# Kernel optimization log

Measured on AMD Instinct MI355X. Metric: run time of the kernel, lower is better.

## Reference

```python
import jax, jax.numpy as jnp
from jax import lax
import numpy as np

RADIUS = 2.0
K = 32          # max_neighbors
KNN = 3         # knn_num for FP interpolation
DEPTH = 3
NH = 16         # nhidden
NIN = 16
NOUT = 2
N = 16384
BOX = 32.0


def sqdist(a, b):
    # a: [M,3], b: [N,3] -> [M,N] squared distances (no [M,N,3] intermediate)
    d2 = (jnp.sum(a * a, -1)[:, None] + jnp.sum(b * b, -1)[None, :]
          - 2.0 * a @ b.T)
    return jnp.maximum(d2, 0.0)


def fps(pos, m):
    # farthest point sampling, deterministic start at index 0 (eval mode)
    n = pos.shape[0]
    def step(carry, _):
        mind, last = carry
        d = jnp.sum((pos - pos[last]) ** 2, axis=-1)
        mind = jnp.minimum(mind, d)
        nxt = jnp.argmax(mind).astype(jnp.int32)
        return (mind, nxt), nxt
    init = (jnp.full((n,), jnp.inf, dtype=pos.dtype), jnp.array(0, jnp.int32))
    _, rest = lax.scan(step, init, None, length=m - 1)
    return jnp.concatenate([jnp.zeros((1,), jnp.int32), rest])


def radius_group(pos_tgt, pos_src, r, k):
    # up-to-k neighbors of each target within radius r (nearest-first)
    d2 = sqdist(pos_tgt, pos_src)                      # [M,N]
    neg = jnp.where(d2 <= r * r, -d2, -jnp.inf)
    vals, cols = lax.top_k(neg, k)                     # [M,K]
    valid = jnp.isfinite(vals)
    return cols, valid


def knn_interpolate(x_c, pos_c, pos_f, k):
    d2 = sqdist(pos_f, pos_c)                          # [Nf, Nc]
    negv, nn = lax.top_k(-d2, k)                       # k nearest coarse pts
    w = 1.0 / jnp.maximum(-negv, 1e-16)
    w = w / jnp.sum(w, -1, keepdims=True)
    return jnp.sum(x_c[nn] * w[..., None], axis=1)     # [Nf, C]


def mlp2(h, W0, b0, W1, b1, act_last=True):
    h = jax.nn.relu(h @ W0 + b0)
    h = h @ W1 + b1
    return jax.nn.relu(h) if act_last else h


def setup_inputs() -> dict:
    key = jax.random.key(0)
    ks = jax.random.split(key, 24)
    s = 0.2
    dim_sa = NH + 3   # 19: PointConv concat(x_j, rel_pos)
    dim_fp = NH + NH  # 32: FP concat(interp, skip)
    return {
        "x": jax.random.normal(ks[0], (N, NIN), jnp.float32),
        "pos": jax.random.uniform(ks[1], (N, 3), jnp.float32) * BOX,
        "batch": jnp.zeros((N,), jnp.int32),
        "lin_in_W0": jax.random.normal(ks[2], (NIN, NH)) * s,
        "lin_in_b0": jnp.zeros((NH,), jnp.float32),
        "lin_in_W1": jax.random.normal(ks[3], (NH, NH)) * s,
        "lin_in_b1": jnp.zeros((NH,), jnp.float32),
        "sa_W0": jax.random.normal(ks[4], (DEPTH, dim_sa, dim_sa)) * s,
        "sa_b0": jnp.zeros((DEPTH, dim_sa), jnp.float32),
        "sa_W1": jax.random.normal(ks[5], (DEPTH, dim_sa, NH)) * s,
        "sa_b1": jnp.zeros((DEPTH, NH), jnp.float32),
        "fp_W0": jax.random.normal(ks[6], (DEPTH, dim_fp, dim_fp)) * s,
        "fp_b0": jnp.zeros((DEPTH, dim_fp), jnp.float32),
        "fp_W1": jax.random.normal(ks[7], (DEPTH, dim_fp, NH)) * s,
        "fp_b1": jnp.zeros((DEPTH, NH), jnp.float32),
        "lo_W0": jax.random.normal(ks[8], (NH, NH)) * s,
        "lo_b0": jnp.zeros((NH,), jnp.float32),
        "lo_W1": jax.random.normal(ks[9], (NH, NOUT)) * s,
        "lo_b1": jnp.zeros((NOUT,), jnp.float32),
    }


def reference(x, pos, batch,
              lin_in_W0, lin_in_b0, lin_in_W1, lin_in_b1,
              sa_W0, sa_b0, sa_W1, sa_b1,
              fp_W0, fp_b0, fp_W1, fp_b1,
              lo_W0, lo_b0, lo_W1, lo_b1):
    # lin_in MLP
    h = mlp2(x, lin_in_W0, lin_in_b0, lin_in_W1, lin_in_b1)
    sa = [(h, pos)]
    # SA (downsampling) path
    for i in range(DEPTH):
        xi, pi = sa[i]
        m = pi.shape[0] // 2                      # ratio = 0.5
        idx = fps(pi, m)
        pt = pi[idx]                              # sampled centers [M,3]
        cols, valid = radius_group(pt, pi, RADIUS, K)   # [M,K]
        xj = xi[cols]                             # [M,K,NH]
        rel = pi[cols] - pt[:, None, :]           # [M,K,3]
        msg = jnp.concatenate([xj, rel], -1)      # [M,K,19]
        msg = mlp2(msg, sa_W0[i], sa_b0[i], sa_W1[i], sa_b1[i])
        msg = jnp.where(valid[..., None], msg, -1e30)
        xn = jnp.max(msg, axis=1)                 # max aggregation (PointConv)
        sa.append((xn, pt))
    # FP (upsampling) path
    xf, pf = sa[DEPTH]
    for i in range(DEPTH - 1, -1, -1):
        xs, ps = sa[i]
        xi = knn_interpolate(xf, pf, ps, KNN)
        hcat = jnp.concatenate([xi, xs], -1)      # [Nf, 32]
        xf = mlp2(hcat, fp_W0[i], fp_b0[i], fp_W1[i], fp_b1[i])
        pf = ps
    # lin_out: relu then linear (act=['relu', None])
    return mlp2(xf, lo_W0, lo_b0, lo_W1, lo_b1, act_last=False)
```

## Files before the change

kernel.cpp:

```cpp
#include <hip/hip_runtime.h>
#include <stdint.h>


#define DEV static __device__ __forceinline__

DEV float fadd_(float a, float b){ return __fadd_rn(a,b); }
DEV float fsub_(float a, float b){ return __fsub_rn(a,b); }
DEV float fmul_(float a, float b){ return __fmul_rn(a,b); }
DEV float fdiv_(float a, float b){ return __fdiv_rn(a,b); }

DEV float dot3(float ax,float ay,float az,float bx,float by,float bz){
  return fmaf(az,bz, fmaf(ay,by, __fmul_rn(ax,bx)));
}
DEV float sqd(float na, float nb, float d){
  float t = __fadd_rn(na, nb);
  float u = __fmul_rn(2.0f, d);
  return fmaxf(__fsub_rn(t, u), 0.0f);
}

DEV float bbd2(float sx,float sy,float sz,
               float lx,float ly,float lz,float hx,float hy,float hz){
  float dx = fmaxf(fmaxf(fsub_(lx,sx), fsub_(sx,hx)), 0.0f);
  float dy = fmaxf(fmaxf(fsub_(ly,sy), fsub_(sy,hy)), 0.0f);
  float dz = fmaxf(fmaxf(fsub_(lz,sz), fsub_(sz,hz)), 0.0f);
  return fadd_(fadd_(fmul_(dx,dx),fmul_(dy,dy)),fmul_(dz,dz));
}

#define DPP0(src, ctrl, rm, bc) \
  __builtin_amdgcn_update_dpp(0, (int)(src), (ctrl), (rm), 0xf, (bc))

#define DPP64(dst, src, ctrl, rm, bc) { \
  uint32_t lo_ = (uint32_t)DPP0((uint32_t)(src), ctrl, rm, bc); \
  uint32_t hi_ = (uint32_t)DPP0((uint32_t)((src)>>32), ctrl, rm, bc); \
  (dst) = (((unsigned long long)hi_)<<32) | lo_; }

#define MERGE2(A1, A2, ctrl, rm, bc) { \
  unsigned long long b1_, b2_, mn_, mx_; \
  DPP64(b1_, A1, ctrl, rm, bc); \
  DPP64(b2_, A2, ctrl, rm, bc); \
  mn_ = (A1) < b1_ ? (A1) : b1_; \
  mx_ = (A2) > b2_ ? (A2) : b2_; \
  (A1) = (A1) > b1_ ? (A1) : b1_; \
  (A2) = mn_ > mx_ ? mn_ : mx_; }

DEV unsigned long long rdlane64(unsigned long long v, int l){
  uint32_t lo=(uint32_t)__builtin_amdgcn_readlane((int)(uint32_t)v, l);
  uint32_t hi=(uint32_t)__builtin_amdgcn_readlane((int)(uint32_t)(v>>32), l);
  return (((unsigned long long)hi)<<32)|lo;
}

DEV void wtop2(unsigned long long &A1, unsigned long long &A2){
  MERGE2(A1,A2,0x111,0xf,true)
  MERGE2(A1,A2,0x112,0xf,true)
  MERGE2(A1,A2,0x114,0xf,true)
  MERGE2(A1,A2,0x118,0xf,true)
  MERGE2(A1,A2,0x142,0xa,false)
  MERGE2(A1,A2,0x143,0xc,false)
  A1 = rdlane64(A1,63); A2 = rdlane64(A2,63);
}
DEV void htop2(unsigned long long &A1, unsigned long long &A2){
  MERGE2(A1,A2,0x111,0xf,true)
  MERGE2(A1,A2,0x112,0xf,true)
  MERGE2(A1,A2,0x114,0xf,true)
  MERGE2(A1,A2,0x118,0xf,true)
  MERGE2(A1,A2,0x142,0xa,false)
  A1 = rdlane64(A1,31); A2 = rdlane64(A2,31);
}

__global__ __launch_bounds__(256) void k_prep(
    const float* __restrict__ x, const float* __restrict__ pos,
    const float* __restrict__ W0, const float* __restrict__ b0,
    const float* __restrict__ W1, const float* __restrict__ b1,
    float4* __restrict__ pos4, float* __restrict__ h_out, int n)
{
  __shared__ float sW0[256], sb0[16], sW1[256], sb1[16];
  int tid = threadIdx.x;
  sW0[tid] = W0[tid];
  sW1[tid] = W1[tid];
  if (tid < 16){ sb0[tid] = b0[tid]; sb1[tid] = b1[tid]; }
  __syncthreads();
  int p = blockIdx.x*256 + tid;
  if (p >= n) return;

  float px = pos[3*p], py = pos[3*p+1], pz = pos[3*p+2];
  float nrm = fadd_(fadd_(fmul_(px,px), fmul_(py,py)), fmul_(pz,pz));
  pos4[p] = make_float4(px,py,pz,nrm);

  const float4* xr = (const float4*)(x + (size_t)p*16);
  float4 v0 = xr[0], v1 = xr[1], v2 = xr[2], v3 = xr[3];
  float xin[16] = {v0.x,v0.y,v0.z,v0.w, v1.x,v1.y,v1.z,v1.w,
                   v2.x,v2.y,v2.z,v2.w, v3.x,v3.y,v3.z,v3.w};
  float h1[16];
  #pragma unroll
  for (int o=0;o<16;o++){
    float acc = fmul_(xin[0], sW0[o]);
    #pragma unroll
    for (int k=1;k<16;k++) acc = fmaf(xin[k], sW0[k*16+o], acc);
    h1[o] = fmaxf(fadd_(acc, sb0[o]), 0.0f);
  }
  float h2[16];
  #pragma unroll
  for (int o=0;o<16;o++){
    float acc = fmul_(h1[0], sW1[o]);
    #pragma unroll
    for (int k=1;k<16;k++) acc = fmaf(h1[k], sW1[k*16+o], acc);
    h2[o] = fmaxf(fadd_(acc, sb1[o]), 0.0f);
  }
  float4* hw = (float4*)(h_out + (size_t)p*16);
  hw[0] = make_float4(h2[0], h2[1], h2[2], h2[3]);
  hw[1] = make_float4(h2[4], h2[5], h2[6], h2[7]);
  hw[2] = make_float4(h2[8], h2[9], h2[10],h2[11]);
  hw[3] = make_float4(h2[12],h2[13],h2[14],h2[15]);
}

DEV uint32_t expand4(uint32_t v){
  return (v&1u) | ((v&2u)<<2) | ((v&4u)<<4) | ((v&8u)<<6);
}
DEV int cellc(float v){
  int c = (int)(v*0.5f);
  return c < 0 ? 0 : (c > 15 ? 15 : c);
}
DEV uint32_t mkey(float4 p){
  return expand4((uint32_t)cellc(p.x))
       | (expand4((uint32_t)cellc(p.y))<<1)
       | (expand4((uint32_t)cellc(p.z))<<2);
}

__global__ __launch_bounds__(1024) void k_sort(
  const float4* __restrict__ nat, float4* __restrict__ srt,
  int* __restrict__ rank0, int n)
{
  __shared__ uint32_t hist[4096];
  __shared__ uint32_t gsum[1024];
  int tid = threadIdx.x;
  for (int i=tid;i<4096;i+=1024) hist[i]=0u;
  __syncthreads();
  for (int i=tid;i<n;i+=1024){
    float4 p = nat[i];
    atomicAdd(&hist[mkey(p)], 1u);
  }
  __syncthreads();
  uint32_t h0=hist[4*tid],h1=hist[4*tid+1],h2=hist[4*tid+2],h3=hist[4*tid+3];
  gsum[tid] = h0+h1+h2+h3;
  __syncthreads();
  for (int off=1; off<1024; off<<=1){
    uint32_t v = gsum[tid];
    uint32_t a = (tid>=off)? gsum[tid-off] : 0u;
    __syncthreads();
    gsum[tid] = v + a;
    __syncthreads();
  }
  uint32_t excl = (tid>0)? gsum[tid-1] : 0u;
  hist[4*tid]   = excl;
  hist[4*tid+1] = excl + h0;
  hist[4*tid+2] = excl + h0 + h1;
  hist[4*tid+3] = excl + h0 + h1 + h2;
  __syncthreads();
  for (int i=tid;i<n;i+=1024){
    float4 p = nat[i];
    uint32_t r = atomicAdd(&hist[mkey(p)], 1u);
    srt[r] = make_float4(p.x, p.y, p.z, __uint_as_float((uint32_t)i));
    if (i==0) *rank0 = (int)r;
  }
}

template<int P>
__global__ __launch_bounds__(1024,4) void k_fps4(
    const float4* __restrict__ sp4,
    const int* __restrict__ rank0p,
    float4* __restrict__ samp,
    int m)
{
  __shared__ float smind[P*1024];
  __shared__ uint32_t xch[2][32*5];
  const int t = threadIdx.x;
  const int lane = t & 63;
  const int w = t >> 6;

  float px[P], py[P], pz[P];
  uint32_t klo[P];
  float blox,bloy,bloz,bhix,bhiy,bhiz;
  #pragma unroll
  for (int k=0;k<P;k++){
    float4 p = sp4[t*P+k];
    px[k]=p.x; py[k]=p.y; pz[k]=p.z;
    uint32_t nat = __float_as_uint(p.w);
    klo[k] = ((0x3FFFu - nat)<<16) | (uint32_t)(t*P+k);
    smind[k*1024+t] = __builtin_inff();
    if (k==0){ blox=bhix=p.x; bloy=bhiy=p.y; bloz=bhiz=p.z; }
    else {
      blox=fminf(blox,p.x); bhix=fmaxf(bhix,p.x);
      bloy=fminf(bloy,p.y); bhiy=fmaxf(bhiy,p.y);
      bloz=fminf(bloz,p.z); bhiz=fmaxf(bhiz,p.z);
    }
  }

  float c1x,c1y,c1z, c2x=0.f,c2y=0.f,c2z=0.f;
  {
    int r0 = *rank0p;
    float4 s0 = sp4[r0];
    c1x=s0.x; c1y=s0.y; c1z=s0.z;
    if (t==0){
      float nr = fadd_(fadd_(fmul_(s0.x,s0.x),fmul_(s0.y,s0.y)),fmul_(s0.z,s0.z));
      samp[0] = make_float4(s0.x,s0.y,s0.z,nr);
    }
  }
  __syncthreads();

  unsigned long long tc1 = ((unsigned long long)0x7f800000u)<<32, tc2 = 0ull;
  bool own1 = false, own2 = false;
  uint32_t c1lo=0,c1hi=0, c2lo=0,c2hi=0;
  float o1x=0,o1y=0,o1z=0, o2x=0,o2y=0,o2z=0;

  int u2 = 0, sel = 1, round = 0;

  while (true){
    bool updp;
    {
      float cv = __uint_as_float((uint32_t)(tc1>>32));
      float dm = bbd2(c1x,c1y,c1z, blox,bloy,bloz,bhix,bhiy,bhiz);
      if (u2){
        float dd = bbd2(c2x,c2y,c2z, blox,bloy,bloz,bhix,bhiy,bhiz);
        dm = fminf(dm, dd);
      }
      updp = (fmul_(dm, 0.99999f) < cv);
    }
    if (__ballot(updp) != 0ull){
      if (updp){
        tc1 = 0ull; tc2 = 0ull;
        #pragma unroll
        for (int k=0;k<P;k++){
          float dx=fsub_(px[k],c1x), dy=fsub_(py[k],c1y), dz=fsub_(pz[k],c1z);
          float da = fadd_(fadd_(fmul_(dx,dx),fmul_(dy,dy)),fmul_(dz,dz));
          float nm = fminf(smind[k*1024+t], da);
          if (u2){
            float ex=fsub_(px[k],c2x), ey=fsub_(py[k],c2y), ez=fsub_(pz[k],c2z);
            float db = fadd_(fadd_(fmul_(ex,ex),fmul_(ey,ey)),fmul_(ez,ez));
            nm = fminf(nm, db);
          }
          smind[k*1024+t] = nm;
          unsigned long long key =
            (((unsigned long long)__float_as_uint(nm))<<32) | klo[k];
          bool g1 = key > tc1;
          unsigned long long nt2 = g1 ? tc1 : (key > tc2 ? key : tc2);
          tc1 = g1 ? key : tc1;
          tc2 = nt2;
        }
      }
      unsigned long long a1 = tc1, a2 = tc2;
      wtop2(a1, a2);
      own1 = (tc1 == a1);
      own2 = (tc1 == a2) || (tc2 == a2);
      int kk1 = (int)(a1 & (unsigned long long)(P-1));
      int kk2 = (int)(a2 & (unsigned long long)(P-1));
      float sx1=px[0], sy1=py[0], sz1=pz[0];
      float sx2=px[0], sy2=py[0], sz2=pz[0];
      #pragma unroll
      for (int j=1;j<P;j++){
        bool e1=(j==kk1), e2=(j==kk2);
        sx1=e1?px[j]:sx1; sy1=e1?py[j]:sy1; sz1=e1?pz[j]:sz1;
        sx2=e2?px[j]:sx2; sy2=e2?py[j]:sy2; sz2=e2?pz[j]:sz2;
      }
      c1lo=(uint32_t)a1; c1hi=(uint32_t)(a1>>32); o1x=sx1; o1y=sy1; o1z=sz1;
      c2lo=(uint32_t)a2; c2hi=(uint32_t)(a2>>32); o2x=sx2; o2y=sy2; o2z=sz2;
    }
    int par = round & 1;
    if (own1){
      int b = (w*2)*5;
      xch[par][b]=c1lo; xch[par][b+1]=c1hi;
      xch[par][b+2]=__float_as_uint(o1x);
      xch[par][b+3]=__float_as_uint(o1y);
      xch[par][b+4]=__float_as_uint(o1z);
    }
    if (own2){
      int b = (w*2+1)*5;
      xch[par][b]=c2lo; xch[par][b+1]=c2hi;
      xch[par][b+2]=__float_as_uint(o2x);
      xch[par][b+3]=__float_as_uint(o2y);
      xch[par][b+4]=__float_as_uint(o2z);
    }
    __syncthreads();
    unsigned long long cnd = 0ull;
    if (lane < 32){
      uint32_t lo = xch[par][lane*5], hi = xch[par][lane*5+1];
      cnd = (((unsigned long long)hi)<<32) | lo;
    }
    unsigned long long a1 = cnd, a2 = 0ull;
    htop2(a1, a2);
    unsigned long long b1 = __ballot(lane<32 && cnd==a1);
    unsigned long long b2 = __ballot(lane<32 && cnd==a2);
    int s1 = __ffsll(b1)-1;
    int s2 = __ffsll(b2)-1;
    float p1x=__uint_as_float(xch[par][s1*5+2]);
    float p1y=__uint_as_float(xch[par][s1*5+3]);
    float p1z=__uint_as_float(xch[par][s1*5+4]);
    float p2x=__uint_as_float(xch[par][s2*5+2]);
    float p2y=__uint_as_float(xch[par][s2*5+3]);
    float p2z=__uint_as_float(xch[par][s2*5+4]);
    float v2 = __uint_as_float((uint32_t)(a2>>32));
    float qx=fsub_(p2x,p1x), qy=fsub_(p2y,p1y), qz=fsub_(p2z,p1z);
    float q  = fadd_(fadd_(fmul_(qx,qx),fmul_(qy,qy)),fmul_(qz,qz));
    bool acc2 = (sel+1 < m) && (q >= v2);
    if (t==0){
      float nr = fadd_(fadd_(fmul_(p1x,p1x),fmul_(p1y,p1y)),fmul_(p1z,p1z));
      samp[sel] = make_float4(p1x,p1y,p1z,nr);
    }
    if (acc2 && t==1){
      float nr = fadd_(fadd_(fmul_(p2x,p2x),fmul_(p2y,p2y)),fmul_(p2z,p2z));
      samp[sel+1] = make_float4(p2x,p2y,p2z,nr);
    }
    sel += acc2 ? 2 : 1;
    round++;
    if (sel >= m) break;
    c1x=p1x; c1y=p1y; c1z=p1z;
    u2 = acc2 ? 1 : 0;
    if (acc2){ c2x=p2x; c2y=p2y; c2z=p2z; }
  }
}

#define SA_CAP 96

__global__ __launch_bounds__(256) void k_sa(
  const float4* __restrict__ spos, int n_src,
  const float4* __restrict__ tpos,
  const float*  __restrict__ F,
  const float* __restrict__ W0, const float* __restrict__ b0,
  const float* __restrict__ W1, const float* __restrict__ b1,
  float* __restrict__ Fout)
{
  __shared__ float sW0[361], sb0[19], sW1[304], sb1[16];
  __shared__ int   nidx[4][SA_CAP];
  __shared__ float nd2[4][SA_CAP];
  int tid = threadIdx.x;
  for (int i=tid;i<361;i+=256) sW0[i]=W0[i];
  for (int i=tid;i<304;i+=256) sW1[i]=W1[i];
  if (tid<19) sb0[tid]=b0[tid];
  if (tid<16) sb1[tid]=b1[tid];
  __syncthreads();

  int wv = tid >> 6, lane = tid & 63;
  int tg = blockIdx.x*4 + wv;
  float4 tp = tpos[tg];

  int cnt = 0;
  for (int base=0; base<n_src; base+=64){
    int j = base + lane;
    float4 sp = spos[j];
    float d2 = sqd(tp.w, sp.w, dot3(tp.x,tp.y,tp.z, sp.x,sp.y,sp.z));
    bool in = (d2 <= 4.0f);
    unsigned long long mk = __ballot(in);
    int pos = cnt + __popcll(mk & ((1ull<<lane)-1ull));
    if (in && pos < SA_CAP){ nidx[wv][pos]=j; nd2[wv][pos]=d2; }
    cnt += __popcll(mk);
  }
  if (cnt > SA_CAP) cnt = SA_CAP;

  if (cnt > 32){
    uint64_t tk0=0, tk1=0;
    for (int r=0;r<32;r++){
      float bvv = 3.5e38f; int bii = 0x7fffffff; int be = 0;
      for (int e=0;e<cnt;e++){
        bool done = (e<64) ? ((tk0>>e)&1ull) : ((tk1>>(e-64))&1ull);
        if (done) continue;
        float dv = nd2[wv][e]; int di = nidx[wv][e];
        if (dv < bvv || (dv == bvv && di < bii)){ bvv=dv; bii=di; be=e; }
      }
      if (be < 64) tk0 |= (1ull<<be); else tk1 |= (1ull<<(be-64));
    }
    int myi = 0; float myd = 0.0f;
    if (lane < 32){
      int seen = 0, sel = -1;
      for (int e=0;e<cnt && sel<0;e++){
        bool s = (e<64) ? ((tk0>>e)&1ull) : ((tk1>>(e-64))&1ull);
        if (s){ if (seen == lane) sel = e; seen++; }
      }
      myi = nidx[wv][sel]; myd = nd2[wv][sel];
    }
    __builtin_amdgcn_wave_barrier();
    if (lane < 32){ nidx[wv][lane]=myi; nd2[wv][lane]=myd; }
    __builtin_amdgcn_wave_barrier();
    cnt = 32;
  }

  float in19[19];
  #pragma unroll
  for (int k=0;k<19;k++) in19[k] = 0.0f;
  if (lane < cnt){
    int j = nidx[wv][lane];
    const float4* fr = (const float4*)(F + (size_t)j*16);
    float4 a=fr[0], b=fr[1], c=fr[2], d=fr[3];
    in19[0]=a.x; in19[1]=a.y; in19[2]=a.z; in19[3]=a.w;
    in19[4]=b.x; in19[5]=b.y; in19[6]=b.z; in19[7]=b.w;
    in19[8]=c.x; in19[9]=c.y; in19[10]=c.z; in19[11]=c.w;
    in19[12]=d.x; in19[13]=d.y; in19[14]=d.z; in19[15]=d.w;
    float4 sp = spos[j];
    in19[16]=fsub_(sp.x,tp.x); in19[17]=fsub_(sp.y,tp.y); in19[18]=fsub_(sp.z,tp.z);
  }
  float h[19];
  #pragma unroll
  for (int o=0;o<19;o++){
    float acc = fmul_(in19[0], sW0[o]);
    #pragma unroll
    for (int k=1;k<19;k++) acc = fmaf(in19[k], sW0[k*19+o], acc);
    h[o] = fmaxf(fadd_(acc, sb0[o]), 0.0f);
  }
  float outv[16];
  #pragma unroll
  for (int o=0;o<16;o++){
    float acc = fmul_(h[0], sW1[o]);
    #pragma unroll
    for (int k=1;k<19;k++) acc = fmaf(h[k], sW1[k*16+o], acc);
    float v = fmaxf(fadd_(acc, sb1[o]), 0.0f);
    outv[o] = (lane < cnt) ? v : -1e30f;
  }
  #pragma unroll
  for (int o=0;o<16;o++){
    float v = outv[o];
    #pragma unroll
    for (int s=1;s<64;s<<=1) v = fmaxf(v, __shfl_xor(v, s));
    outv[o] = v;
  }
  if (lane == 0){
    float4* dst = (float4*)(Fout + (size_t)tg*16);
    dst[0] = make_float4(outv[0], outv[1], outv[2], outv[3]);
    dst[1] = make_float4(outv[4], outv[5], outv[6], outv[7]);
    dst[2] = make_float4(outv[8], outv[9], outv[10],outv[11]);
    dst[3] = make_float4(outv[12],outv[13],outv[14],outv[15]);
  }
}
// ... 98 lines not shown
    if (lane < 2) outp[(size_t)f*2 + lane] = a4;
  }
}

extern "C" void kernel_launch(void* const* d_in, const int* in_sizes, int n_in,
                              void* d_out, int out_size, void* d_ws, size_t ws_size,
                              hipStream_t stream) {
  (void)in_sizes; (void)n_in; (void)out_size; (void)ws_size;
  const float* x     = (const float*)d_in[0];
  const float* pos   = (const float*)d_in[1];
  const float* liW0  = (const float*)d_in[3];
  const float* lib0  = (const float*)d_in[4];
  const float* liW1  = (const float*)d_in[5];
  const float* lib1  = (const float*)d_in[6];
  const float* saW0  = (const float*)d_in[7];
  const float* sab0  = (const float*)d_in[8];
  const float* saW1  = (const float*)d_in[9];
  const float* sab1  = (const float*)d_in[10];
  const float* fpW0  = (const float*)d_in[11];
  const float* fpb0  = (const float*)d_in[12];
  const float* fpW1  = (const float*)d_in[13];
  const float* fpb1  = (const float*)d_in[14];
  const float* loW0  = (const float*)d_in[15];
  const float* lob0  = (const float*)d_in[16];
  const float* loW1  = (const float*)d_in[17];
  const float* lob1  = (const float*)d_in[18];
  float* out = (float*)d_out;

  char* ws = (char*)d_ws;
  size_t off = 0;
  auto alloc = [&](size_t bytes)->void* {
    void* p = ws + off;
    off += (bytes + 255) & ~(size_t)255;
    return p;
  };
  float4* P0 = (float4*)alloc(16384u*16);
  float4* P1 = (float4*)alloc(8192u*16);
  float4* P2 = (float4*)alloc(4096u*16);
  float4* P3 = (float4*)alloc(2048u*16);
  float*  F0 = (float*)alloc(16384u*16*4);
  float*  F1 = (float*)alloc(8192u*16*4);
  float*  F2 = (float*)alloc(4096u*16*4);
  float*  F3 = (float*)alloc(2048u*16*4);
  float*  G2 = (float*)alloc(4096u*16*4);
  float*  G1 = (float*)alloc(8192u*16*4);
  float4* S0 = (float4*)alloc(16384u*16);
  float4* S1 = (float4*)alloc(8192u*16);
  float4* S2 = (float4*)alloc(4096u*16);
  int*    R0 = (int*)alloc(256);

  k_prep<<<64,256,0,stream>>>(x,pos, liW0,lib0,liW1,lib1, P0,F0, 16384);

  k_sort<<<1,1024,0,stream>>>(P0, S0, R0+0, 16384);
  k_fps4<16><<<1,1024,0,stream>>>(S0, R0+0, P1, 8192);
  k_sa<<<2048,256,0,stream>>>(P0,16384, P1, F0, saW0,      sab0,    saW1,      sab1,    F1);
  k_sort<<<1,1024,0,stream>>>(P1, S1, R0+1, 8192);
  k_fps4<8><<<1,1024,0,stream>>>(S1, R0+1, P2, 4096);
  k_sa<<<1024,256,0,stream>>>(P1, 8192, P2, F1, saW0+361,  sab0+19, saW1+304,  sab1+16, F2);
  k_sort<<<1,1024,0,stream>>>(P2, S2, R0+2, 4096);
  k_fps4<4><<<1,1024,0,stream>>>(S2, R0+2, P3, 2048);
  k_sa<<< 512,256,0,stream>>>(P2, 4096, P3, F2, saW0+722,  sab0+38, saW1+608,  sab1+32, F3);

  k_fp<<<1024,256,0,stream>>>(P2, P3,2048, F3, F2,
      fpW0+2048, fpb0+64, fpW1+1024, fpb1+32,
      loW0,lob0,loW1,lob1, G2, 0);
  k_fp<<<2048,256,0,stream>>>(P1, P2,4096, G2, F1,
      fpW0+1024, fpb0+32, fpW1+512,  fpb1+16,
      loW0,lob0,loW1,lob1, G1, 0);
  k_fp<<<4096,256,0,stream>>>(P0, P1,8192, G1, F0,
      fpW0,      fpb0,    fpW1,      fpb1,
      loW0,lob0,loW1,lob1, out, 1);
}
```

Baseline: 20.59 ms.

## Accept up to six FPS samples per round instead of two

The farthest-point-sampling kernel now gathers up to six candidates per block-wide round. It repeatedly takes the next-best per-wave candidate and accepts it only if its distance to every already accepted candidate in that round is at least its own min-distance, which keeps the sequence identical to plain FPS. The min-distance update then applies all accepted centers in one pass over the point registers. The goal is fewer serial rounds, each with its own syncthreads and cross-wave reduction, in a kernel that runs on a single block. In exchange each round does more serial wave reductions and more register work, and the stopping rule when the chosen slot is odd (only two candidates per wave are stored) limits how many samples a round can accept.

```diff
diff --git a/kernel.cpp b/kernel.cpp
--- a/kernel.cpp
+++ b/kernel.cpp
@@ -58,13 +58,16 @@
   MERGE2(A1,A2,0x143,0xc,false)
   A1 = rdlane64(A1,63); A2 = rdlane64(A2,63);
 }
-DEV void htop2(unsigned long long &A1, unsigned long long &A2){
-  MERGE2(A1,A2,0x111,0xf,true)
-  MERGE2(A1,A2,0x112,0xf,true)
-  MERGE2(A1,A2,0x114,0xf,true)
-  MERGE2(A1,A2,0x118,0xf,true)
-  MERGE2(A1,A2,0x142,0xa,false)
-  A1 = rdlane64(A1,31); A2 = rdlane64(A2,31);
+
+DEV unsigned long long wmax64b(unsigned long long v){
+  unsigned long long b;
+  DPP64(b,v,0x111,0xf,true)  v = v>b?v:b;
+  DPP64(b,v,0x112,0xf,true)  v = v>b?v:b;
+  DPP64(b,v,0x114,0xf,true)  v = v>b?v:b;
+  DPP64(b,v,0x118,0xf,true)  v = v>b?v:b;
+  DPP64(b,v,0x142,0xa,false) v = v>b?v:b;
+  DPP64(b,v,0x143,0xc,false) v = v>b?v:b;
+  return rdlane64(v,63);
 }
 
 __global__ __launch_bounds__(256) void k_prep(
@@ -164,8 +167,10 @@
   }
 }
 
+#define KACC 6
+
 template<int P>
-__global__ __launch_bounds__(1024,4) void k_fps4(
+__global__ __launch_bounds__(1024) void k_fps6(
     const float4* __restrict__ sp4,
     const int* __restrict__ rank0p,
     float4* __restrict__ samp,
@@ -195,11 +200,14 @@
     }
   }
 
-  float c1x,c1y,c1z, c2x=0.f,c2y=0.f,c2z=0.f;
+  float ax[KACC], ay[KACC], az[KACC];
+  int u = 1;
   {
     int r0 = *rank0p;
     float4 s0 = sp4[r0];
-    c1x=s0.x; c1y=s0.y; c1z=s0.z;
+    ax[0]=s0.x; ay[0]=s0.y; az[0]=s0.z;
+    #pragma unroll
+    for (int j=1;j<KACC;j++){ ax[j]=0.f; ay[j]=0.f; az[j]=0.f; }
     if (t==0){
       float nr = fadd_(fadd_(fmul_(s0.x,s0.x),fmul_(s0.y,s0.y)),fmul_(s0.z,s0.z));
       samp[0] = make_float4(s0.x,s0.y,s0.z,nr);
@@ -212,35 +220,47 @@
   uint32_t c1lo=0,c1hi=0, c2lo=0,c2hi=0;
   float o1x=0,o1y=0,o1z=0, o2x=0,o2y=0,o2z=0;
 
-  int u2 = 0, sel = 1, round = 0;
+  int sel = 1, round = 0;
 
   while (true){
     bool updp;
     {
       float cv = __uint_as_float((uint32_t)(tc1>>32));
-      float dm = bbd2(c1x,c1y,c1z, blox,bloy,bloz,bhix,bhiy,bhiz);
-      if (u2){
-        float dd = bbd2(c2x,c2y,c2z, blox,bloy,bloz,bhix,bhiy,bhiz);
-        dm = fminf(dm, dd);
+      float dm = bbd2(ax[0],ay[0],az[0], blox,bloy,bloz,bhix,bhiy,bhiz);
+      #pragma unroll
+      for (int j=1;j<KACC;j++){
+        if (j < u){
+          float dd = bbd2(ax[j],ay[j],az[j], blox,bloy,bloz,bhix,bhiy,bhiz);
+          dm = fminf(dm, dd);
+        }
       }
       updp = (fmul_(dm, 0.99999f) < cv);
     }
     if (__ballot(updp) != 0ull){
       if (updp){
+        float nm[P];
+        #pragma unroll
+        for (int k=0;k<P;k++) nm[k] = smind[k*1024+t];
+        for (int j=0;j<u;j++){
+          float cx=ax[0], cy=ay[0], cz=az[0];
+          #pragma unroll
+          for (int q=1;q<KACC;q++){
+            bool e = (q==j);
+            cx = e?ax[q]:cx; cy = e?ay[q]:cy; cz = e?az[q]:cz;
+          }
+          #pragma unroll
+          for (int k=0;k<P;k++){
+            float dx=fsub_(px[k],cx), dy=fsub_(py[k],cy), dz=fsub_(pz[k],cz);
+            float d2 = fadd_(fadd_(fmul_(dx,dx),fmul_(dy,dy)),fmul_(dz,dz));
+            nm[k] = fminf(nm[k], d2);
+          }
+        }
         tc1 = 0ull; tc2 = 0ull;
         #pragma unroll
         for (int k=0;k<P;k++){
-          float dx=fsub_(px[k],c1x), dy=fsub_(py[k],c1y), dz=fsub_(pz[k],c1z);
-          float da = fadd_(fadd_(fmul_(dx,dx),fmul_(dy,dy)),fmul_(dz,dz));
-          float nm = fminf(smind[k*1024+t], da);
-          if (u2){
-            float ex=fsub_(px[k],c2x), ey=fsub_(py[k],c2y), ez=fsub_(pz[k],c2z);
-            float db = fadd_(fadd_(fmul_(ex,ex),fmul_(ey,ey)),fmul_(ez,ez));
-            nm = fminf(nm, db);
-          }
-          smind[k*1024+t] = nm;
+          smind[k*1024+t] = nm[k];
           unsigned long long key =
-            (((unsigned long long)__float_as_uint(nm))<<32) | klo[k];
+            (((unsigned long long)__float_as_uint(nm[k]))<<32) | klo[k];
           bool g1 = key > tc1;
           unsigned long long nt2 = g1 ? tc1 : (key > tc2 ? key : tc2);
           tc1 = g1 ? key : tc1;
@@ -285,36 +305,47 @@
       uint32_t lo = xch[par][lane*5], hi = xch[par][lane*5+1];
       cnd = (((unsigned long long)hi)<<32) | lo;
     }
-    unsigned long long a1 = cnd, a2 = 0ull;
-    htop2(a1, a2);
-    unsigned long long b1 = __ballot(lane<32 && cnd==a1);
-    unsigned long long b2 = __ballot(lane<32 && cnd==a2);
-    int s1 = __ffsll(b1)-1;
-    int s2 = __ffsll(b2)-1;
-    float p1x=__uint_as_float(xch[par][s1*5+2]);
-    float p1y=__uint_as_float(xch[par][s1*5+3]);
-    float p1z=__uint_as_float(xch[par][s1*5+4]);
-    float p2x=__uint_as_float(xch[par][s2*5+2]);
-    float p2y=__uint_as_float(xch[par][s2*5+3]);
-    float p2z=__uint_as_float(xch[par][s2*5+4]);
-    float v2 = __uint_as_float((uint32_t)(a2>>32));
-    float qx=fsub_(p2x,p1x), qy=fsub_(p2y,p1y), qz=fsub_(p2z,p1z);
-    float q  = fadd_(fadd_(fmul_(qx,qx),fmul_(qy,qy)),fmul_(qz,qz));
-    bool acc2 = (sel+1 < m) && (q >= v2);
-    if (t==0){
-      float nr = fadd_(fadd_(fmul_(p1x,p1x),fmul_(p1y,p1y)),fmul_(p1z,p1z));
-      samp[sel] = make_float4(p1x,p1y,p1z,nr);
-    }
-    if (acc2 && t==1){
-      float nr = fadd_(fadd_(fmul_(p2x,p2x),fmul_(p2y,p2y)),fmul_(p2z,p2z));
-      samp[sel+1] = make_float4(p2x,p2y,p2z,nr);
-    }
-    sel += acc2 ? 2 : 1;
+    int unew = 0;
+    bool stop = false;
+    #pragma unroll
+    for (int i=0;i<KACC;i++){
+      if (!stop){
+        if (i > 0 && !(sel + i < m)){
+          stop = true;
+        } else {
+          unsigned long long mx = wmax64b(cnd);
+          unsigned long long bal = __ballot(cnd == mx);
+          int s = __ffsll((unsigned long long)bal) - 1;
+          float cxx = __uint_as_float(xch[par][s*5+2]);
+          float cyy = __uint_as_float(xch[par][s*5+3]);
+          float czz = __uint_as_float(xch[par][s*5+4]);
+          float v   = __uint_as_float((uint32_t)(mx>>32));
+          bool ok = true;
+          #pragma unroll
+          for (int j=0;j<i;j++){
+            float dx=fsub_(cxx,ax[j]), dy=fsub_(cyy,ay[j]), dz=fsub_(czz,az[j]);
+            float d2 = fadd_(fadd_(fmul_(dx,dx),fmul_(dy,dy)),fmul_(dz,dz));
+            ok = ok && (d2 >= v);
+          }
+          if (i > 0 && !ok){
+            stop = true;
+          } else {
+            ax[i]=cxx; ay[i]=cyy; az[i]=czz;
+            unew = i + 1;
+            if (t == 0){
+              float nr = fadd_(fadd_(fmul_(cxx,cxx),fmul_(cyy,cyy)),fmul_(czz,czz));
+              samp[sel + i] = make_float4(cxx,cyy,czz,nr);
+            }
+            cnd = (cnd == mx) ? 0ull : cnd;
+            if (s & 1) stop = true;
+          }
+        }
+      }
+    }
+    sel += unew;
+    u = unew;
     round++;
     if (sel >= m) break;
-    c1x=p1x; c1y=p1y; c1z=p1z;
-    u2 = acc2 ? 1 : 0;
-    if (acc2){ c2x=p2x; c2y=p2y; c2z=p2z; }
   }
 }
 
@@ -369,12 +400,12 @@
     }
     int myi = 0; float myd = 0.0f;
     if (lane < 32){
-      int seen = 0, sel = -1;
-      for (int e=0;e<cnt && sel<0;e++){
+      int seen = 0, sl = -1;
+      for (int e=0;e<cnt && sl<0;e++){
         bool s = (e<64) ? ((tk0>>e)&1ull) : ((tk1>>(e-64))&1ull);
-        if (s){ if (seen == lane) sel = e; seen++; }
+        if (s){ if (seen == lane) sl = e; seen++; }
       }
-      myi = nidx[wv][sel]; myd = nd2[wv][sel];
+      myi = nidx[wv][sl]; myd = nd2[wv][sl];
     }
     __builtin_amdgcn_wave_barrier();
     if (lane < 32){ nidx[wv][lane]=myi; nd2[wv][lane]=myd; }
@@ -579,13 +610,13 @@
   k_prep<<<64,256,0,stream>>>(x,pos, liW0,lib0,liW1,lib1, P0,F0, 16384);
 
   k_sort<<<1,1024,0,stream>>>(P0, S0, R0+0, 16384);
-  k_fps4<16><<<1,1024,0,stream>>>(S0, R0+0, P1, 8192);
+  k_fps6<16><<<1,1024,0,stream>>>(S0, R0+0, P1, 8192);
   k_sa<<<2048,256,0,stream>>>(P0,16384, P1, F0, saW0,      sab0,    saW1,      sab1,    F1);
   k_sort<<<1,1024,0,stream>>>(P1, S1, R0+1, 8192);
-  k_fps4<8><<<1,1024,0,stream>>>(S1, R0+1, P2, 4096);
+  k_fps6<8><<<1,1024,0,stream>>>(S1, R0+1, P2, 4096);
   k_sa<<<1024,256,0,stream>>>(P1, 8192, P2, F1, saW0+361,  sab0+19, saW1+304,  sab1+16, F2);
   k_sort<<<1,1024,0,stream>>>(P2, S2, R0+2, 4096);
-  k_fps4<4><<<1,1024,0,stream>>>(S2, R0+2, P3, 2048);
+  k_fps6<4><<<1,1024,0,stream>>>(S2, R0+2, P3, 2048);
   k_sa<<< 512,256,0,stream>>>(P2, 4096, P3, F2, saW0+722,  sab0+38, saW1+608,  sab1+32, F3);
 
   k_fp<<<1024,256,0,stream>>>(P2, P3,2048, F3, F2,
```

After: 23.98 ms. 16.5% more time.

## Restructure FPS kernel to 512 threads with register mind and sub-box culling

Applied to the files above, without the earlier changes.

The single-block farthest point sampling kernel now runs with 512 threads (8 waves) instead of 1024, holding twice as many points per thread, with the running min-distance kept in registers instead of shared memory. Each thread's points are split into sub-groups with their own bounding boxes, so only sub-groups the new centers can affect are recomputed, and the top-2 candidates carry their coordinates along, which removes the per-round select loop. The cross-wave exchange shrinks to 16 candidates, making the per-round reduction shorter. The cost is higher register pressure (waves_per_eu 2) and fewer threads doing distance work per round.

```diff
diff --git a/kernel.cpp b/kernel.cpp
--- a/kernel.cpp
+++ b/kernel.cpp
@@ -58,13 +58,12 @@
   MERGE2(A1,A2,0x143,0xc,false)
   A1 = rdlane64(A1,63); A2 = rdlane64(A2,63);
 }
-DEV void htop2(unsigned long long &A1, unsigned long long &A2){
+DEV void qtop2(unsigned long long &A1, unsigned long long &A2){
   MERGE2(A1,A2,0x111,0xf,true)
   MERGE2(A1,A2,0x112,0xf,true)
   MERGE2(A1,A2,0x114,0xf,true)
   MERGE2(A1,A2,0x118,0xf,true)
-  MERGE2(A1,A2,0x142,0xa,false)
-  A1 = rdlane64(A1,31); A2 = rdlane64(A2,31);
+  A1 = rdlane64(A1,15); A2 = rdlane64(A2,15);
 }
 
 __global__ __launch_bounds__(256) void k_prep(
@@ -165,34 +164,47 @@
 }
 
 template<int P>
-__global__ __launch_bounds__(1024,4) void k_fps4(
+__global__ __attribute__((amdgpu_waves_per_eu(2,2)))
+__launch_bounds__(512) void k_fps8(
     const float4* __restrict__ sp4,
     const int* __restrict__ rank0p,
     float4* __restrict__ samp,
     int m)
 {
-  __shared__ float smind[P*1024];
-  __shared__ uint32_t xch[2][32*5];
+  constexpr int SUBS = (P >= 32) ? (P/16) : 1;
+  constexpr int SZ   = P / SUBS;
+  __shared__ uint32_t xch[2][16*5];
   const int t = threadIdx.x;
   const int lane = t & 63;
   const int w = t >> 6;
 
-  float px[P], py[P], pz[P];
+  float px[P], py[P], pz[P], mind[P];
   uint32_t klo[P];
-  float blox,bloy,bloz,bhix,bhiy,bhiz;
+  float sblx[SUBS],sbly[SUBS],sblz[SUBS],sbhx[SUBS],sbhy[SUBS],sbhz[SUBS];
+  unsigned long long sp1[SUBS], sp2[SUBS];
+  float s1x[SUBS],s1y[SUBS],s1z[SUBS],s2x[SUBS],s2y[SUBS],s2z[SUBS];
+
   #pragma unroll
   for (int k=0;k<P;k++){
     float4 p = sp4[t*P+k];
     px[k]=p.x; py[k]=p.y; pz[k]=p.z;
-    uint32_t nat = __float_as_uint(p.w);
-    klo[k] = ((0x3FFFu - nat)<<16) | (uint32_t)(t*P+k);
-    smind[k*1024+t] = __builtin_inff();
-    if (k==0){ blox=bhix=p.x; bloy=bhiy=p.y; bloz=bhiz=p.z; }
-    else {
-      blox=fminf(blox,p.x); bhix=fmaxf(bhix,p.x);
-      bloy=fminf(bloy,p.y); bhiy=fmaxf(bhiy,p.y);
-      bloz=fminf(bloz,p.z); bhiz=fmaxf(bhiz,p.z);
-    }
+    mind[k] = __builtin_inff();
+    klo[k] = ((0x3FFFu - __float_as_uint(p.w))<<16) | (uint32_t)(t*P+k);
+    int s = k / SZ;
+    if ((k % SZ) == 0){
+      sblx[s]=p.x; sbhx[s]=p.x; sbly[s]=p.y; sbhy[s]=p.y; sblz[s]=p.z; sbhz[s]=p.z;
+    } else {
+      sblx[s]=fminf(sblx[s],p.x); sbhx[s]=fmaxf(sbhx[s],p.x);
+      sbly[s]=fminf(sbly[s],p.y); sbhy[s]=fmaxf(sbhy[s],p.y);
+      sblz[s]=fminf(sblz[s],p.z); sbhz[s]=fmaxf(sbhz[s],p.z);
+    }
+  }
+  #pragma unroll
+  for (int s=0;s<SUBS;s++){
+    sp1[s] = ((unsigned long long)0x7f800000u)<<32;
+    sp2[s] = 0ull;
+    s1x[s]=px[s*SZ]; s1y[s]=py[s*SZ]; s1z[s]=pz[s*SZ];
+    s2x[s]=px[s*SZ]; s2y[s]=py[s*SZ]; s2z[s]=pz[s*SZ];
   }
 
   float c1x,c1y,c1z, c2x=0.f,c2y=0.f,c2z=0.f;
@@ -205,90 +217,120 @@
       samp[0] = make_float4(s0.x,s0.y,s0.z,nr);
     }
   }
-  __syncthreads();
-
-  unsigned long long tc1 = ((unsigned long long)0x7f800000u)<<32, tc2 = 0ull;
+
   bool own1 = false, own2 = false;
-  uint32_t c1lo=0,c1hi=0, c2lo=0,c2hi=0;
+  uint32_t p1lo=0,p1hi=0, p2lo=0,p2hi=0;
   float o1x=0,o1y=0,o1z=0, o2x=0,o2y=0,o2z=0;
 
   int u2 = 0, sel = 1, round = 0;
 
   while (true){
-    bool updp;
-    {
-      float cv = __uint_as_float((uint32_t)(tc1>>32));
-      float dm = bbd2(c1x,c1y,c1z, blox,bloy,bloz,bhix,bhiy,bhiz);
+    bool sdirty[SUBS]; bool updp = false;
+    #pragma unroll
+    for (int s=0;s<SUBS;s++){
+      float dm = bbd2(c1x,c1y,c1z, sblx[s],sbly[s],sblz[s],sbhx[s],sbhy[s],sbhz[s]);
       if (u2){
-        float dd = bbd2(c2x,c2y,c2z, blox,bloy,bloz,bhix,bhiy,bhiz);
+        float dd = bbd2(c2x,c2y,c2z, sblx[s],sbly[s],sblz[s],sbhx[s],sbhy[s],sbhz[s]);
         dm = fminf(dm, dd);
       }
-      updp = (fmul_(dm, 0.99999f) < cv);
+      sdirty[s] = (fmul_(dm, 0.99999f) < __uint_as_float((uint32_t)(sp1[s]>>32)));
+      updp |= sdirty[s];
     }
     if (__ballot(updp) != 0ull){
       if (updp){
-        tc1 = 0ull; tc2 = 0ull;
         #pragma unroll
-        for (int k=0;k<P;k++){
-          float dx=fsub_(px[k],c1x), dy=fsub_(py[k],c1y), dz=fsub_(pz[k],c1z);
-          float da = fadd_(fadd_(fmul_(dx,dx),fmul_(dy,dy)),fmul_(dz,dz));
-          float nm = fminf(smind[k*1024+t], da);
-          if (u2){
-            float ex=fsub_(px[k],c2x), ey=fsub_(py[k],c2y), ez=fsub_(pz[k],c2z);
-            float db = fadd_(fadd_(fmul_(ex,ex),fmul_(ey,ey)),fmul_(ez,ez));
-            nm = fminf(nm, db);
+        for (int s=0;s<SUBS;s++){
+          if (sdirty[s]){
+            unsigned long long q1 = 0ull, q2 = 0ull;
+            float a1x=px[s*SZ],a1y=py[s*SZ],a1z=pz[s*SZ];
+            float a2xx=px[s*SZ],a2yy=py[s*SZ],a2zz=pz[s*SZ];
+            #pragma unroll
+            for (int q=0;q<SZ;q++){
+              const int k = s*SZ+q;
+              float dx=fsub_(px[k],c1x), dy=fsub_(py[k],c1y), dz=fsub_(pz[k],c1z);
+              float da = fadd_(fadd_(fmul_(dx,dx),fmul_(dy,dy)),fmul_(dz,dz));
+              float nm = fminf(mind[k], da);
+              if (u2){
+                float ex=fsub_(px[k],c2x), ey=fsub_(py[k],c2y), ez=fsub_(pz[k],c2z);
+                float db = fadd_(fadd_(fmul_(ex,ex),fmul_(ey,ey)),fmul_(ez,ez));
+                nm = fminf(nm, db);
+              }
+              mind[k] = nm;
+              unsigned long long key =
+                (((unsigned long long)__float_as_uint(nm))<<32) | klo[k];
+              bool g1 = key > q1;
+              bool g2 = key > q2;
+              unsigned long long nq2 = g1 ? q1 : (g2 ? key : q2);
+              float n2x = g1 ? a1x : (g2 ? px[k] : a2xx);
+              float n2y = g1 ? a1y : (g2 ? py[k] : a2yy);
+              float n2z = g1 ? a1z : (g2 ? pz[k] : a2zz);
+              q1 = g1 ? key : q1;
+              a1x = g1 ? px[k] : a1x;
+              a1y = g1 ? py[k] : a1y;
+              a1z = g1 ? pz[k] : a1z;
+              q2 = nq2; a2xx = n2x; a2yy = n2y; a2zz = n2z;
+            }
+            sp1[s]=q1; sp2[s]=q2;
+            s1x[s]=a1x; s1y[s]=a1y; s1z[s]=a1z;
+            s2x[s]=a2xx; s2y[s]=a2yy; s2z[s]=a2zz;
           }
-          smind[k*1024+t] = nm;
-          unsigned long long key =
-            (((unsigned long long)__float_as_uint(nm))<<32) | klo[k];
-          bool g1 = key > tc1;
-          unsigned long long nt2 = g1 ? tc1 : (key > tc2 ? key : tc2);
-          tc1 = g1 ? key : tc1;
-          tc2 = nt2;
         }
       }
-      unsigned long long a1 = tc1, a2 = tc2;
+      unsigned long long m1 = sp1[0], m2 = sp2[0];
+      float m1x=s1x[0],m1y=s1y[0],m1z=s1z[0];
+      float m2xx=s2x[0],m2yy=s2y[0],m2zz=s2z[0];
+      #pragma unroll
+      for (int s=1;s<SUBS;s++){
+        unsigned long long b1 = sp1[s], b2 = sp2[s];
+        bool bg = b1 > m1;
+        unsigned long long mn = bg ? m1 : b1;
+        float mnx = bg ? m1x : s1x[s], mny = bg ? m1y : s1y[s], mnz = bg ? m1z : s1z[s];
+        bool xg = m2 > b2;
+        unsigned long long mx = xg ? m2 : b2;
+        float mxx = xg ? m2xx : s2x[s], mxy = xg ? m2yy : s2y[s], mxz = xg ? m2zz : s2z[s];
+        m1 = bg ? b1 : m1;
+        m1x = bg ? s1x[s] : m1x; m1y = bg ? s1y[s] : m1y; m1z = bg ? s1z[s] : m1z;
+        bool sg = mn > mx;
+        m2 = sg ? mn : mx;
+        m2xx = sg ? mnx : mxx; m2yy = sg ? mny : mxy; m2zz = sg ? mnz : mxz;
+      }
+      unsigned long long a1 = m1, a2 = m2;
       wtop2(a1, a2);
-      own1 = (tc1 == a1);
-      own2 = (tc1 == a2) || (tc2 == a2);
-      int kk1 = (int)(a1 & (unsigned long long)(P-1));
-      int kk2 = (int)(a2 & (unsigned long long)(P-1));
-      float sx1=px[0], sy1=py[0], sz1=pz[0];
-      float sx2=px[0], sy2=py[0], sz2=pz[0];
-      #pragma unroll
-      for (int j=1;j<P;j++){
-        bool e1=(j==kk1), e2=(j==kk2);
-        sx1=e1?px[j]:sx1; sy1=e1?py[j]:sy1; sz1=e1?pz[j]:sz1;
-        sx2=e2?px[j]:sx2; sy2=e2?py[j]:sy2; sz2=e2?pz[j]:sz2;
-      }
-      c1lo=(uint32_t)a1; c1hi=(uint32_t)(a1>>32); o1x=sx1; o1y=sy1; o1z=sz1;
-      c2lo=(uint32_t)a2; c2hi=(uint32_t)(a2>>32); o2x=sx2; o2y=sy2; o2z=sz2;
+      own1 = (m1 == a1);
+      own2 = (m1 == a2) || (m2 == a2);
+      bool from1 = (m1 == a2);
+      p1lo=(uint32_t)a1; p1hi=(uint32_t)(a1>>32);
+      o1x=m1x; o1y=m1y; o1z=m1z;
+      p2lo=(uint32_t)a2; p2hi=(uint32_t)(a2>>32);
+      o2x = from1 ? m1x : m2xx;
+      o2y = from1 ? m1y : m2yy;
+      o2z = from1 ? m1z : m2zz;
     }
     int par = round & 1;
     if (own1){
       int b = (w*2)*5;
-      xch[par][b]=c1lo; xch[par][b+1]=c1hi;
+      xch[par][b]=p1lo; xch[par][b+1]=p1hi;
       xch[par][b+2]=__float_as_uint(o1x);
       xch[par][b+3]=__float_as_uint(o1y);
       xch[par][b+4]=__float_as_uint(o1z);
     }
     if (own2){
       int b = (w*2+1)*5;
-      xch[par][b]=c2lo; xch[par][b+1]=c2hi;
+      xch[par][b]=p2lo; xch[par][b+1]=p2hi;
       xch[par][b+2]=__float_as_uint(o2x);
       xch[par][b+3]=__float_as_uint(o2y);
       xch[par][b+4]=__float_as_uint(o2z);
     }
     __syncthreads();
     unsigned long long cnd = 0ull;
-    if (lane < 32){
+    if (lane < 16){
       uint32_t lo = xch[par][lane*5], hi = xch[par][lane*5+1];
       cnd = (((unsigned long long)hi)<<32) | lo;
     }
     unsigned long long a1 = cnd, a2 = 0ull;
-    htop2(a1, a2);
-    unsigned long long b1 = __ballot(lane<32 && cnd==a1);
-    unsigned long long b2 = __ballot(lane<32 && cnd==a2);
+    qtop2(a1, a2);
+    unsigned long long b1 = __ballot(lane<16 && cnd==a1);
+    unsigned long long b2 = __ballot(lane<16 && cnd==a2);
     int s1 = __ffsll(b1)-1;
     int s2 = __ffsll(b2)-1;
     float p1x=__uint_as_float(xch[par][s1*5+2]);
@@ -369,12 +411,12 @@
     }
     int myi = 0; float myd = 0.0f;
     if (lane < 32){
-      int seen = 0, sel = -1;
-      for (int e=0;e<cnt && sel<0;e++){
+      int seen = 0, sl = -1;
+      for (int e=0;e<cnt && sl<0;e++){
         bool s = (e<64) ? ((tk0>>e)&1ull) : ((tk1>>(e-64))&1ull);
-        if (s){ if (seen == lane) sel = e; seen++; }
+        if (s){ if (seen == lane) sl = e; seen++; }
       }
-      myi = nidx[wv][sel]; myd = nd2[wv][sel];
+      myi = nidx[wv][sl]; myd = nd2[wv][sl];
     }
     __builtin_amdgcn_wave_barrier();
     if (lane < 32){ nidx[wv][lane]=myi; nd2[wv][lane]=myd; }
@@ -579,13 +621,13 @@
   k_prep<<<64,256,0,stream>>>(x,pos, liW0,lib0,liW1,lib1, P0,F0, 16384);
 
   k_sort<<<1,1024,0,stream>>>(P0, S0, R0+0, 16384);
-  k_fps4<16><<<1,1024,0,stream>>>(S0, R0+0, P1, 8192);
+  k_fps8<32><<<1,512,0,stream>>>(S0, R0+0, P1, 8192);
   k_sa<<<2048,256,0,stream>>>(P0,16384, P1, F0, saW0,      sab0,    saW1,      sab1,    F1);
   k_sort<<<1,1024,0,stream>>>(P1, S1, R0+1, 8192);
-  k_fps4<8><<<1,1024,0,stream>>>(S1, R0+1, P2, 4096);
+  k_fps8<16><<<1,512,0,stream>>>(S1, R0+1, P2, 4096);
   k_sa<<<1024,256,0,stream>>>(P1, 8192, P2, F1, saW0+361,  sab0+19, saW1+304,  sab1+16, F2);
   k_sort<<<1,1024,0,stream>>>(P2, S2, R0+2, 4096);
-  k_fps4<4><<<1,1024,0,stream>>>(S2, R0+2, P3, 2048);
+  k_fps8<8><<<1,512,0,stream>>>(S2, R0+2, P3, 2048);
   k_sa<<< 512,256,0,stream>>>(P2, 4096, P3, F2, saW0+722,  sab0+38, saW1+608,  sab1+32, F3);
 
   k_fp<<<1024,256,0,stream>>>(P2, P3,2048, F3, F2,
```

Result: slower. 27.80 ms (+35.0%).

## Accept up to eight FPS samples per round via speculative candidate validation

Applied to the files above, without the earlier changes.

The farthest-point-sampling kernel used to accept at most two new samples per block-wide round. It now gathers the top-2 candidates from each of the 16 waves (32 in total) and has one wave rank them and check their pairwise distances. It then accepts the longest prefix of up to 8 candidates that are provably the true sequential FPS choices, and broadcasts them through shared memory for the next distance update. This cuts the number of serial rounds and __syncthreads barriers, which dominate this single-block kernel. The cost is extra per-round distance work for K centers and a heavier selection step, and the prefix is limited because only two candidates per wave are seen.

```diff
diff --git a/kernel.cpp b/kernel.cpp
--- a/kernel.cpp
+++ b/kernel.cpp
@@ -57,14 +57,6 @@
   MERGE2(A1,A2,0x142,0xa,false)
   MERGE2(A1,A2,0x143,0xc,false)
   A1 = rdlane64(A1,63); A2 = rdlane64(A2,63);
-}
-DEV void htop2(unsigned long long &A1, unsigned long long &A2){
-  MERGE2(A1,A2,0x111,0xf,true)
-  MERGE2(A1,A2,0x112,0xf,true)
-  MERGE2(A1,A2,0x114,0xf,true)
-  MERGE2(A1,A2,0x118,0xf,true)
-  MERGE2(A1,A2,0x142,0xa,false)
-  A1 = rdlane64(A1,31); A2 = rdlane64(A2,31);
 }
 
 __global__ __launch_bounds__(256) void k_prep(
@@ -165,14 +157,16 @@
 }
 
 template<int P>
-__global__ __launch_bounds__(1024,4) void k_fps4(
+__global__ __launch_bounds__(1024) void k_fps10(
     const float4* __restrict__ sp4,
     const int* __restrict__ rank0p,
     float4* __restrict__ samp,
     int m)
 {
   __shared__ float smind[P*1024];
-  __shared__ uint32_t xch[2][32*5];
+  __shared__ uint32_t xch[32*5];
+  __shared__ float4 cbuf[8];
+  __shared__ uint32_t resK;
   const int t = threadIdx.x;
   const int lane = t & 63;
   const int w = t >> 6;
@@ -195,32 +189,30 @@
     }
   }
 
-  float c1x,c1y,c1z, c2x=0.f,c2y=0.f,c2z=0.f;
   {
     int r0 = *rank0p;
     float4 s0 = sp4[r0];
-    c1x=s0.x; c1y=s0.y; c1z=s0.z;
     if (t==0){
       float nr = fadd_(fadd_(fmul_(s0.x,s0.x),fmul_(s0.y,s0.y)),fmul_(s0.z,s0.z));
       samp[0] = make_float4(s0.x,s0.y,s0.z,nr);
+      cbuf[0] = make_float4(s0.x,s0.y,s0.z,0.f);
+      resK = 1u;
     }
   }
   __syncthreads();
 
   unsigned long long tc1 = ((unsigned long long)0x7f800000u)<<32, tc2 = 0ull;
-  bool own1 = false, own2 = false;
-  uint32_t c1lo=0,c1hi=0, c2lo=0,c2hi=0;
-  float o1x=0,o1y=0,o1z=0, o2x=0,o2y=0,o2z=0;
-
-  int u2 = 0, sel = 1, round = 0;
+  int sel = 1;
 
   while (true){
+    const int K = (int)resK;
     bool updp;
     {
       float cv = __uint_as_float((uint32_t)(tc1>>32));
-      float dm = bbd2(c1x,c1y,c1z, blox,bloy,bloz,bhix,bhiy,bhiz);
-      if (u2){
-        float dd = bbd2(c2x,c2y,c2z, blox,bloy,bloz,bhix,bhiy,bhiz);
+      float dm = 3.5e38f;
+      for (int r=0;r<K;r++){
+        float4 c = cbuf[r];
+        float dd = bbd2(c.x,c.y,c.z, blox,bloy,bloz,bhix,bhiy,bhiz);
         dm = fminf(dm, dd);
       }
       updp = (fmul_(dm, 0.99999f) < cv);
@@ -230,13 +222,12 @@
         tc1 = 0ull; tc2 = 0ull;
         #pragma unroll
         for (int k=0;k<P;k++){
-          float dx=fsub_(px[k],c1x), dy=fsub_(py[k],c1y), dz=fsub_(pz[k],c1z);
-          float da = fadd_(fadd_(fmul_(dx,dx),fmul_(dy,dy)),fmul_(dz,dz));
-          float nm = fminf(smind[k*1024+t], da);
-          if (u2){
-            float ex=fsub_(px[k],c2x), ey=fsub_(py[k],c2y), ez=fsub_(pz[k],c2z);
-            float db = fadd_(fadd_(fmul_(ex,ex),fmul_(ey,ey)),fmul_(ez,ez));
-            nm = fminf(nm, db);
+          float nm = smind[k*1024+t];
+          for (int r=0;r<K;r++){
+            float4 c = cbuf[r];
+            float dx=fsub_(px[k],c.x), dy=fsub_(py[k],c.y), dz=fsub_(pz[k],c.z);
+            float d2 = fadd_(fadd_(fmul_(dx,dx),fmul_(dy,dy)),fmul_(dz,dz));
+            nm = fminf(nm, d2);
           }
           smind[k*1024+t] = nm;
           unsigned long long key =
@@ -249,8 +240,8 @@
       }
       unsigned long long a1 = tc1, a2 = tc2;
       wtop2(a1, a2);
-      own1 = (tc1 == a1);
-      own2 = (tc1 == a2) || (tc2 == a2);
+      bool own1 = (tc1 == a1);
+      bool own2 = (tc1 == a2) || (tc2 == a2);
       int kk1 = (int)(a1 & (unsigned long long)(P-1));
       int kk2 = (int)(a2 & (unsigned long long)(P-1));
       float sx1=px[0], sy1=py[0], sz1=pz[0];
@@ -261,60 +252,70 @@
         sx1=e1?px[j]:sx1; sy1=e1?py[j]:sy1; sz1=e1?pz[j]:sz1;
         sx2=e2?px[j]:sx2; sy2=e2?py[j]:sy2; sz2=e2?pz[j]:sz2;
       }
-      c1lo=(uint32_t)a1; c1hi=(uint32_t)(a1>>32); o1x=sx1; o1y=sy1; o1z=sz1;
-      c2lo=(uint32_t)a2; c2hi=(uint32_t)(a2>>32); o2x=sx2; o2y=sy2; o2z=sz2;
-    }
-    int par = round & 1;
-    if (own1){
-      int b = (w*2)*5;
-      xch[par][b]=c1lo; xch[par][b+1]=c1hi;
-      xch[par][b+2]=__float_as_uint(o1x);
-      xch[par][b+3]=__float_as_uint(o1y);
-      xch[par][b+4]=__float_as_uint(o1z);
-    }
-    if (own2){
-      int b = (w*2+1)*5;
-      xch[par][b]=c2lo; xch[par][b+1]=c2hi;
-      xch[par][b+2]=__float_as_uint(o2x);
-      xch[par][b+3]=__float_as_uint(o2y);
-      xch[par][b+4]=__float_as_uint(o2z);
+      if (own1){
+        int b = (w*2)*5;
+        xch[b]  =(uint32_t)a1; xch[b+1]=(uint32_t)(a1>>32);
+        xch[b+2]=__float_as_uint(sx1);
+        xch[b+3]=__float_as_uint(sy1);
+        xch[b+4]=__float_as_uint(sz1);
+      }
+      if (own2){
+        int b = (w*2+1)*5;
+        xch[b]  =(uint32_t)a2; xch[b+1]=(uint32_t)(a2>>32);
+        xch[b+2]=__float_as_uint(sx2);
+        xch[b+3]=__float_as_uint(sy2);
+        xch[b+4]=__float_as_uint(sz2);
+      }
     }
     __syncthreads();
-    unsigned long long cnd = 0ull;
-    if (lane < 32){
-      uint32_t lo = xch[par][lane*5], hi = xch[par][lane*5+1];
-      cnd = (((unsigned long long)hi)<<32) | lo;
-    }
-    unsigned long long a1 = cnd, a2 = 0ull;
-    htop2(a1, a2);
-    unsigned long long b1 = __ballot(lane<32 && cnd==a1);
-    unsigned long long b2 = __ballot(lane<32 && cnd==a2);
-    int s1 = __ffsll(b1)-1;
-    int s2 = __ffsll(b2)-1;
-    float p1x=__uint_as_float(xch[par][s1*5+2]);
-    float p1y=__uint_as_float(xch[par][s1*5+3]);
-    float p1z=__uint_as_float(xch[par][s1*5+4]);
-    float p2x=__uint_as_float(xch[par][s2*5+2]);
-    float p2y=__uint_as_float(xch[par][s2*5+3]);
-    float p2z=__uint_as_float(xch[par][s2*5+4]);
-    float v2 = __uint_as_float((uint32_t)(a2>>32));
-    float qx=fsub_(p2x,p1x), qy=fsub_(p2y,p1y), qz=fsub_(p2z,p1z);
-    float q  = fadd_(fadd_(fmul_(qx,qx),fmul_(qy,qy)),fmul_(qz,qz));
-    bool acc2 = (sel+1 < m) && (q >= v2);
-    if (t==0){
-      float nr = fadd_(fadd_(fmul_(p1x,p1x),fmul_(p1y,p1y)),fmul_(p1z,p1z));
-      samp[sel] = make_float4(p1x,p1y,p1z,nr);
-    }
-    if (acc2 && t==1){
-      float nr = fadd_(fadd_(fmul_(p2x,p2x),fmul_(p2y,p2y)),fmul_(p2z,p2z));
-      samp[sel+1] = make_float4(p2x,p2y,p2z,nr);
-    }
-    sel += acc2 ? 2 : 1;
-    round++;
+    if (t < 64){
+      const int j = lane & 31;
+      const int half = lane >> 5;
+      uint32_t kjlo = xch[j*5], kjhi = xch[j*5+1];
+      unsigned long long kj = (((unsigned long long)kjhi)<<32) | kjlo;
+      float cjx = __uint_as_float(xch[j*5+2]);
+      float cjy = __uint_as_float(xch[j*5+3]);
+      float cjz = __uint_as_float(xch[j*5+4]);
+      float vj  = __uint_as_float(kjhi);
+      int rankc = 0; int okc = 1;
+      #pragma unroll
+      for (int i0=0;i0<16;i0++){
+        int i = half*16 + i0;
+        uint32_t kilo = xch[i*5], kihi = xch[i*5+1];
+        unsigned long long ki = (((unsigned long long)kihi)<<32) | kilo;
+        float cix = __uint_as_float(xch[i*5+2]);
+        float ciy = __uint_as_float(xch[i*5+3]);
+        float ciz = __uint_as_float(xch[i*5+4]);
+        if (ki > kj){
+          rankc++;
+          float dx=fsub_(cjx,cix), dy=fsub_(cjy,ciy), dz=fsub_(cjz,ciz);
+          float d2 = fadd_(fadd_(fmul_(dx,dx),fmul_(dy,dy)),fmul_(dz,dz));
+          okc &= (d2 >= vj) ? 1 : 0;
+        }
+      }
+      rankc += __shfl_xor(rankc, 32);
+      okc   &= __shfl_xor(okc, 32);
+      int failr = okc ? 64 : rankc;
+      int twor  = (j & 1) ? (rankc + 1) : 64;
+      #pragma unroll
+      for (int s=1;s<64;s<<=1){
+        int of = __shfl_xor(failr, s); failr = of < failr ? of : failr;
+        int ot = __shfl_xor(twor,  s); twor  = ot < twor  ? ot : twor;
+      }
+      int Knew = failr < twor ? failr : twor;
+      Knew = Knew > 8 ? 8 : Knew;
+      int cap = m - sel;
+      Knew = Knew > cap ? cap : Knew;
+      if (lane < 32 && rankc < Knew){
+        float nr = fadd_(fadd_(fmul_(cjx,cjx),fmul_(cjy,cjy)),fmul_(cjz,cjz));
+        samp[sel + rankc] = make_float4(cjx,cjy,cjz,nr);
+        cbuf[rankc] = make_float4(cjx,cjy,cjz,0.f);
+      }
+      if (lane == 0) resK = (uint32_t)Knew;
+    }
+    __syncthreads();
+    sel += (int)resK;
     if (sel >= m) break;
-    c1x=p1x; c1y=p1y; c1z=p1z;
-    u2 = acc2 ? 1 : 0;
-    if (acc2){ c2x=p2x; c2y=p2y; c2z=p2z; }
   }
 }
 
@@ -369,12 +370,12 @@
     }
     int myi = 0; float myd = 0.0f;
     if (lane < 32){
-      int seen = 0, sel = -1;
-      for (int e=0;e<cnt && sel<0;e++){
+      int seen = 0, sl = -1;
+      for (int e=0;e<cnt && sl<0;e++){
         bool s = (e<64) ? ((tk0>>e)&1ull) : ((tk1>>(e-64))&1ull);
-        if (s){ if (seen == lane) sel = e; seen++; }
-      }
-      myi = nidx[wv][sel]; myd = nd2[wv][sel];
+        if (s){ if (seen == lane) sl = e; seen++; }
+      }
+      myi = nidx[wv][sl]; myd = nd2[wv][sl];
     }
     __builtin_amdgcn_wave_barrier();
     if (lane < 32){ nidx[wv][lane]=myi; nd2[wv][lane]=myd; }
@@ -579,13 +580,13 @@
   k_prep<<<64,256,0,stream>>>(x,pos, liW0,lib0,liW1,lib1, P0,F0, 16384);
 
   k_sort<<<1,1024,0,stream>>>(P0, S0, R0+0, 16384);
-  k_fps4<16><<<1,1024,0,stream>>>(S0, R0+0, P1, 8192);
+  k_fps10<16><<<1,1024,0,stream>>>(S0, R0+0, P1, 8192);
   k_sa<<<2048,256,0,stream>>>(P0,16384, P1, F0, saW0,      sab0,    saW1,      sab1,    F1);
   k_sort<<<1,1024,0,stream>>>(P1, S1, R0+1, 8192);
-  k_fps4<8><<<1,1024,0,stream>>>(S1, R0+1, P2, 4096);
+  k_fps10<8><<<1,1024,0,stream>>>(S1, R0+1, P2, 4096);
   k_sa<<<1024,256,0,stream>>>(P1, 8192, P2, F1, saW0+361,  sab0+19, saW1+304,  sab1+16, F2);
   k_sort<<<1,1024,0,stream>>>(P2, S2, R0+2, 4096);
-  k_fps4<4><<<1,1024,0,stream>>>(S2, R0+2, P3, 2048);
+  k_fps10<4><<<1,1024,0,stream>>>(S2, R0+2, P3, 2048);
   k_sa<<< 512,256,0,stream>>>(P2, 4096, P3, F2, saW0+722,  sab0+38, saW1+608,  sab1+32, F3);
 
   k_fp<<<1024,256,0,stream>>>(P2, P3,2048, F3, F2,
```

After: 35.29 ms. 71.4% more time.
